# Kernel tuning notes

Measured on AMD Instinct MI355X. Metric: run time of the kernel, lower is better.

Reference implementation:

```python
import jax, jax.numpy as jnp
import numpy as np

NUM_HEADS = 8

def conv1x1(x, w, b):
    # x: [B,C,H,W], w: [O,C], b: [O]
    return jnp.einsum('bchw,oc->bohw', x, w) + b[None, :, None, None]

def setup_inputs() -> dict:
    key = jax.random.key(0)
    ks = jax.random.split(key, 8)
    B, C, H, W = 8, 256, 32, 32
    HF, WF = 128, 128
    s = 1.0 / np.sqrt(C)  # xavier-ish scale for 1x1 convs
    return {
        'x': jax.random.normal(ks[0], (B, C, H, W), jnp.float32),
        'featmap': jax.random.normal(ks[1], (B, C, HF, WF), jnp.float32),
        'wq': jax.random.normal(ks[2], (C, C), jnp.float32) * s,
        'bq': jnp.zeros((C,), jnp.float32),
        'wk': jax.random.normal(ks[3], (C, C), jnp.float32) * s,
        'bk': jnp.zeros((C,), jnp.float32),
        'wv': jax.random.normal(ks[4], (C, C), jnp.float32) * s,
        'bv': jnp.zeros((C,), jnp.float32),
        'wg': jax.random.normal(ks[5], (1, C), jnp.float32) * s,
        'bg': jnp.zeros((1,), jnp.float32),
    }

def _to_grid(t, h, w, rh, rw):
    # t: [B8, d, h*rh, w*rw] -> [B8, d, h, w, rh*rw] (aligned local grid per query pixel)
    b8, d = t.shape[:2]
    t = t.reshape(b8, d, h, rh, w, rw)
    return t.transpose(0, 1, 2, 4, 3, 5).reshape(b8, d, h, w, rh * rw)

def reference(x, featmap, wq, bq, wk, bk, wv, bv, wg, bg):
    B, C, H, W = x.shape
    HF, WF = featmap.shape[2:]
    head_dim = C // NUM_HEADS
    scaling = float(head_dim) ** -0.5
    rh, rw = HF // H, WF // W

    grid_weight = jax.nn.sigmoid(conv1x1(x, wg, bg))          # [B,1,H,W]
    q = conv1x1(x, wq, bq) * scaling                           # [B,C,H,W]
    k = conv1x1(featmap, wk, bk)                               # [B,C,HF,WF]
    v = conv1x1(featmap, wv, bv)

    q = q.reshape(B * NUM_HEADS, head_dim, H, W)
    k = k.reshape(B * NUM_HEADS, head_dim, HF, WF)
    v = v.reshape(B * NUM_HEADS, head_dim, HF, WF)

    k_grid = _to_grid(k, H, W, rh, rw)                         # [B8,d,H,W,P]
    v_grid = _to_grid(v, H, W, rh, rw)

    # ga_align_weight: correlate each query pixel with its aligned key grid
    attn = jnp.einsum('bchw,bchwp->bphw', q, k_grid)           # [B8,P,H,W]
    attn = jax.nn.softmax(attn, axis=1)
    # ga_align_map: weighted sum of aligned value grid
    out = jnp.einsum('bphw,bchwp->bchw', attn, v_grid)         # [B8,d,H,W]

    out = out.reshape(B, C, H, W) * grid_weight
    return out
```

## Files before the change

kernel.cpp:

```cpp
#include <hip/hip_runtime.h>

#define CDIM 256
#define SCALING 0.17677669529663687f

typedef _Float16 f16;
typedef f16 f16x4 __attribute__((ext_vector_type(4)));
typedef f16 f16x8 __attribute__((ext_vector_type(8)));
typedef float f32x4 __attribute__((ext_vector_type(4)));

#define MFMA(a, b, c) __builtin_amdgcn_mfma_f32_16x16x32_f16(a, b, c, 0, 0, 0)

__global__ __launch_bounds__(256) void k_prep_w2(const float* __restrict__ wq,
                                                 const float* __restrict__ bq,
                                                 const float* __restrict__ wk,
                                                 f16* __restrict__ W2h,
                                                 float* __restrict__ b2) {
  __shared__ float wk_s[32][8];
  const int t = threadIdx.x, ciO = blockIdx.x, hd = blockIdx.y;
  {
    int j = t >> 3, c8 = t & 7;
    wk_s[j][c8] = wk[(hd * 32 + j) * CDIM + ciO * 8 + c8];
  }
  float wq_r[32];
#pragma unroll
  for (int j = 0; j < 32; ++j) wq_r[j] = wq[(hd * 32 + j) * CDIM + t];
  __syncthreads();
  for (int c8 = 0; c8 < 8; ++c8) {
    float acc = 0.f;
#pragma unroll
    for (int j = 0; j < 32; ++j) acc = fmaf(wq_r[j], wk_s[j][c8], acc);
    W2h[(size_t)(hd * CDIM + ciO * 8 + c8) * CDIM + t] = (f16)(acc * SCALING);
  }
  if (t < 8) {
    float a = 0.f;
    for (int j = 0; j < 32; ++j) a = fmaf(wk_s[j][t], bq[hd * 32 + j], a);
    b2[hd * CDIM + ciO * 8 + t] = a * SCALING;
  }
}

__global__ __launch_bounds__(256) void k_cvt_wv(const float* __restrict__ wv,
                                                f16* __restrict__ wvh) {
  int i = (blockIdx.x * 256 + threadIdx.x) * 4;
  float4 v = *(const float4*)(wv + i);
  f16x4 h;
  h[0] = (f16)v.x; h[1] = (f16)v.y; h[2] = (f16)v.z; h[3] = (f16)v.w;
  *(f16x4*)(wvh + i) = h;
}

__global__ __launch_bounds__(256, 2) void k_qkw2(const float* __restrict__ x,
                                                 const f16* __restrict__ W2h,
                                                 const float* __restrict__ b2,
                                                 const float* __restrict__ wg,
                                                 const float* __restrict__ bg,
                                                 f16* __restrict__ qk,
                                                 float* __restrict__ gw, int b0) {
  __shared__ __align__(16) f16 A_l[256 * 40];
  __shared__ __align__(16) f16 B_l[64 * 40];
  const int t = threadIdx.x;
  const int p16 = blockIdx.x, hd = blockIdx.y, bz = blockIdx.z;
  const int bb = b0 + bz;
  const int lane = t & 63, wid = t >> 6, l15 = lane & 15, h4 = lane >> 4;
  f32x4 acc[4][4] = {};
  float gacc = 0.f;

  for (int kb = 0; kb < 8; ++kb) {
    __syncthreads();
#pragma unroll
    for (int it = 0; it < 4; ++it) {
      int e = it * 256 + t, ci = e >> 2, q = e & 3;
      *(f16x8*)(A_l + ci * 40 + q * 8) =
          *(const f16x8*)(W2h + (size_t)(hd * CDIM + ci) * CDIM + kb * 32 + q * 8);
    }
#pragma unroll
    for (int it = 0; it < 2; ++it) {
      int e = it * 256 + t, cx = e >> 4, p4 = e & 15;
      float4 v = *(const float4*)(x + (size_t)(bb * CDIM + kb * 32 + cx) * 1024 +
                                  p16 * 64 + p4 * 4);
      B_l[(p4 * 4 + 0) * 40 + cx] = (f16)v.x;
      B_l[(p4 * 4 + 1) * 40 + cx] = (f16)v.y;
      B_l[(p4 * 4 + 2) * 40 + cx] = (f16)v.z;
      B_l[(p4 * 4 + 3) * 40 + cx] = (f16)v.w;
    }
    __syncthreads();
    if (hd == 0 && wid == 3) {
#pragma unroll
      for (int cx = 0; cx < 32; ++cx)
        gacc = fmaf(wg[kb * 32 + cx], (float)B_l[lane * 40 + cx], gacc);
    }
    f16x8 a[4], bf[4];
#pragma unroll
    for (int mt = 0; mt < 4; ++mt)
      a[mt] = *(const f16x8*)(A_l + (wid * 64 + mt * 16 + l15) * 40 + h4 * 8);
#pragma unroll
    for (int nt = 0; nt < 4; ++nt)
      bf[nt] = *(const f16x8*)(B_l + (nt * 16 + l15) * 40 + h4 * 8);
#pragma unroll
    for (int mt = 0; mt < 4; ++mt)
#pragma unroll
      for (int nt = 0; nt < 4; ++nt) acc[mt][nt] = MFMA(a[mt], bf[nt], acc[mt][nt]);
  }
#pragma unroll
  for (int mt = 0; mt < 4; ++mt) {
    int ci0 = wid * 64 + mt * 16 + h4 * 4;
    float4 bvv = *(const float4*)(b2 + hd * CDIM + ci0);
#pragma unroll
    for (int nt = 0; nt < 4; ++nt) {
      int pix = p16 * 64 + nt * 16 + l15;
      union { f16 h[4]; unsigned long long u; } P;
      P.h[0] = (f16)(acc[mt][nt][0] + bvv.x);
      P.h[1] = (f16)(acc[mt][nt][1] + bvv.y);
      P.h[2] = (f16)(acc[mt][nt][2] + bvv.z);
      P.h[3] = (f16)(acc[mt][nt][3] + bvv.w);
      *(unsigned long long*)(qk + ((size_t)(bz * 1024 + pix) * 8 + hd) * CDIM + ci0) = P.u;
    }
  }
  if (hd == 0 && wid == 3)
    gw[bz * 1024 + p16 * 64 + lane] = 1.f / (1.f + __expf(-(gacc + bg[0])));
}

__global__ __launch_bounds__(256, 2) void k_attn(const float* __restrict__ feat,
                                                 const f16* __restrict__ qk,
                                                 f16* __restrict__ fa, int b0) {
  __shared__ __align__(16) f16 featb_cip[4 * 4128];
  __shared__ __align__(16) f16 featb_pci[4 * 4224];
  __shared__ __align__(16) f16 attn_l[4 * 16 * 32];
  const int t = threadIdx.x;
  const int h = blockIdx.x, w4 = blockIdx.y, bz = blockIdx.z;
  const int bb = b0 + bz;
  const int lane = t & 63, w = t >> 6, l15 = lane & 15, h4 = lane >> 4;
  const int pixb = h * 32 + w4 * 4;

  {
    f16x8 z = {};
    *(f16x8*)(attn_l + t * 8) = z;
  }
  if (t < 128) {
    int wi = t >> 5, i = t & 31;
    featb_cip[wi * 4128 + 4096 + i] = (f16)0;
  }
  const float* fb = feat + (size_t)bb * (CDIM * 16384) + (h * 4) * 128 + w4 * 16;
#pragma unroll
  for (int it = 0; it < 16; ++it) {
    int e = it * 256 + t, j4 = e & 3, r = (e >> 2) & 3, ci = e >> 4;
    float4 v = *(const float4*)(fb + (size_t)ci * 16384 + r * 128 + j4 * 4);
    f16x4 hv;
    hv[0] = (f16)v.x; hv[1] = (f16)v.y; hv[2] = (f16)v.z; hv[3] = (f16)v.w;
    *(f16x4*)(featb_cip + j4 * 4128 + ci * 16 + r * 4) = hv;
    int pb = j4 * 4224 + ci;
    featb_pci[pb + (r * 4 + 0) * 264] = hv[0];
    featb_pci[pb + (r * 4 + 1) * 264] = hv[1];
    featb_pci[pb + (r * 4 + 2) * 264] = hv[2];
    featb_pci[pb + (r * 4 + 3) * 264] = hv[3];
  }
  __syncthreads();

  const f16* qkg = qk + ((size_t)(bz * 1024 + pixb + w) * 8 + (l15 & 7)) * CDIM;
  const f16* fpci = featb_pci + w * 4224 + l15 * 264;
  f32x4 acc = {};
#pragma unroll
  for (int kb = 0; kb < 8; ++kb) {
    f16x8 a = *(const f16x8*)(qkg + kb * 32 + h4 * 8);
    f16x8 bf = *(const f16x8*)(fpci + kb * 32 + h4 * 8);
    acc = MFMA(a, bf, acc);
  }
  float at[4];
#pragma unroll
  for (int r = 0; r < 4; ++r) {
    float m = acc[r];
    m = fmaxf(m, __shfl_xor(m, 1, 64));
    m = fmaxf(m, __shfl_xor(m, 2, 64));
    m = fmaxf(m, __shfl_xor(m, 4, 64));
    m = fmaxf(m, __shfl_xor(m, 8, 64));
    float e = __expf(acc[r] - m);
    float s = e;
    s += __shfl_xor(s, 1, 64);
    s += __shfl_xor(s, 2, 64);
    s += __shfl_xor(s, 4, 64);
    s += __shfl_xor(s, 8, 64);
    at[r] = e / s;
  }
  if (h4 < 2) {
#pragma unroll
    for (int r = 0; r < 4; ++r) attn_l[(w * 16 + h4 * 4 + r) * 32 + l15] = (f16)at[r];
  }
  f16x8 bfr = *(const f16x8*)(attn_l + (w * 16 + l15) * 32 + h4 * 8);
  const f16* fw = featb_cip + w * 4128;
  f32x4 zero = {};
#pragma unroll
  for (int mt = 0; mt < 16; ++mt) {
    f16x8 a5 = *(const f16x8*)(fw + (mt * 16 + l15) * 16 + h4 * 8);
    f32x4 d = MFMA(a5, bfr, zero);
    if (l15 < 8) {
      int ci0 = mt * 16 + h4 * 4;
      union { f16 h[4]; unsigned long long u; } P;
      P.h[0] = (f16)d[0]; P.h[1] = (f16)d[1]; P.h[2] = (f16)d[2]; P.h[3] = (f16)d[3];
      *(unsigned long long*)(fa + ((size_t)(bz * 8 + l15) * 1024 + pixb + w) * CDIM + ci0) =
          P.u;
    }
  }
}

__global__ __launch_bounds__(256) void k_out(const f16* __restrict__ fa,
                                             const f16* __restrict__ wvh,
                                             const float* __restrict__ bv,
                                             const float* __restrict__ gw,
                                             float* __restrict__ out, int b0) {
  __shared__ __align__(16) f16 wv_l[32 * 264];
  __shared__ __align__(16) f16 fa_l[64 * 40];
  const int t = threadIdx.x;
  const int p16 = blockIdx.x, hd = blockIdx.y, bz = blockIdx.z;
  const int bb = b0 + bz;
  const int lane = t & 63, wid = t >> 6, l15 = lane & 15, h4 = lane >> 4;
#pragma unroll
  for (int it = 0; it < 4; ++it) {
    int e = it * 256 + t, c = e >> 5, ch = e & 31;
    *(f16x8*)(wv_l + c * 264 + ch * 8) =
        *(const f16x8*)(wvh + (size_t)(hd * 32 + c) * CDIM + ch * 8);
  }
  f32x4 acc[2] = {};
  for (int kb = 0; kb < 8; ++kb) {
    __syncthreads();
    {
      int pixl = t >> 2, q = t & 3;
      *(f16x8*)(fa_l + pixl * 40 + q * 8) =
          *(const f16x8*)(fa + ((size_t)(bz * 8 + hd) * 1024 + p16 * 64 + pixl) * CDIM +
                          kb * 32 + q * 8);
    }
    __syncthreads();
    f16x8 a = *(const f16x8*)(fa_l + (wid * 16 + l15) * 40 + h4 * 8);
#pragma unroll
    for (int nt = 0; nt < 2; ++nt) {
      f16x8 b = *(const f16x8*)(wv_l + (nt * 16 + l15) * 264 + kb * 32 + h4 * 8);
      acc[nt] = MFMA(a, b, acc[nt]);
    }
  }
  int pix0 = p16 * 64 + wid * 16 + h4 * 4;
  float4 g = *(const float4*)(gw + bz * 1024 + pix0);
#pragma unroll
  for (int nt = 0; nt < 2; ++nt) {
    int c = hd * 32 + nt * 16 + l15;
    float bvc = bv[c];
    float4 o;
    o.x = (acc[nt][0] + bvc) * g.x;
    o.y = (acc[nt][1] + bvc) * g.y;
    o.z = (acc[nt][2] + bvc) * g.z;
    o.w = (acc[nt][3] + bvc) * g.w;
    *(float4*)(out + (size_t)(bb * CDIM + c) * 1024 + pix0) = o;
  }
}

extern "C" void kernel_launch(void* const* d_in, const int* in_sizes, int n_in,
                              void* d_out, int out_size, void* d_ws, size_t ws_size,
                              hipStream_t stream) {
  const float* x = (const float*)d_in[0];
  const float* feat = (const float*)d_in[1];
  const float* wq = (const float*)d_in[2];
  const float* bq = (const float*)d_in[3];
  const float* wk = (const float*)d_in[4];
  const float* wv = (const float*)d_in[6];
  const float* bv = (const float*)d_in[7];
  const float* wg = (const float*)d_in[8];
  const float* bg = (const float*)d_in[9];
  float* out = (float*)d_out;

  char* ws = (char*)d_ws;
  f16* W2h = (f16*)ws;
  float* b2 = (float*)(ws + 1048576);
  f16* wvh = (f16*)(ws + 1056768);
  char* dyn = ws + 1187840;

  k_prep_w2<<<dim3(32, 8), 256, 0, stream>>>(wq, bq, wk, W2h, b2);
  k_cvt_wv<<<64, 256, 0, stream>>>(wv, wvh);

  const size_t QK = 4194304, FA = 4194304, GW = 4096;
  if (ws_size >= 1187840 + 8 * (QK + FA + GW)) {
    f16* qk = (f16*)dyn;
    f16* fa = (f16*)(dyn + 8 * QK);
    float* gwp = (float*)(dyn + 8 * (QK + FA));
    k_qkw2<<<dim3(16, 8, 8), 256, 0, stream>>>(x, W2h, b2, wg, bg, qk, gwp, 0);
    k_attn<<<dim3(32, 8, 8), 256, 0, stream>>>(feat, qk, fa, 0);
    k_out<<<dim3(16, 8, 8), 256, 0, stream>>>(fa, wvh, bv, gwp, out, 0);
  } else {
    f16* qk = (f16*)dyn;
    f16* fa = (f16*)(dyn + QK);
    float* gwp = (float*)(dyn + QK + FA);
    for (int b = 0; b < 8; ++b) {
      k_qkw2<<<dim3(16, 8, 1), 256, 0, stream>>>(x, W2h, b2, wg, bg, qk, gwp, b);
      k_attn<<<dim3(32, 8, 1), 256, 0, stream>>>(feat, qk, fa, b);
      k_out<<<dim3(16, 8, 1), 256, 0, stream>>>(fa, wvh, bv, gwp, out, b);
    }
  }
}
```

Baseline: 88.21 us.

## Fuse value projection into attention kernel and merge wv conversion into prep

The output 1x1 value projection (k_out) is folded into k_attn. The attention-weighted features stay in shared memory and are multiplied by the f16 wv weights straight from global memory, which removes the fa intermediate write and read round trip. The wv fp32-to-f16 conversion moves into k_prep_w2, which saves a launch. The cost is redundant wv weight reads per block, a strided scalar output store (only 4 lanes write per tile), and MFMA work with mostly idle rows, since only 4 pixels are used per 16-wide tile.

```diff
diff --git a/kernel.cpp b/kernel.cpp
--- a/kernel.cpp
+++ b/kernel.cpp
@@ -13,13 +13,17 @@
 __global__ __launch_bounds__(256) void k_prep_w2(const float* __restrict__ wq,
                                                  const float* __restrict__ bq,
                                                  const float* __restrict__ wk,
+                                                 const float* __restrict__ wv,
                                                  f16* __restrict__ W2h,
-                                                 float* __restrict__ b2) {
+                                                 float* __restrict__ b2,
+                                                 f16* __restrict__ wvh) {
   __shared__ float wk_s[32][8];
   const int t = threadIdx.x, ciO = blockIdx.x, hd = blockIdx.y;
   {
     int j = t >> 3, c8 = t & 7;
     wk_s[j][c8] = wk[(hd * 32 + j) * CDIM + ciO * 8 + c8];
+    int idx = (hd * 32 + j) * CDIM + ciO * 8 + c8;
+    wvh[idx] = (f16)wv[idx];
   }
   float wq_r[32];
 #pragma unroll
@@ -36,15 +40,6 @@
     for (int j = 0; j < 32; ++j) a = fmaf(wk_s[j][t], bq[hd * 32 + j], a);
     b2[hd * CDIM + ciO * 8 + t] = a * SCALING;
   }
-}
-
-__global__ __launch_bounds__(256) void k_cvt_wv(const float* __restrict__ wv,
-                                                f16* __restrict__ wvh) {
-  int i = (blockIdx.x * 256 + threadIdx.x) * 4;
-  float4 v = *(const float4*)(wv + i);
-  f16x4 h;
-  h[0] = (f16)v.x; h[1] = (f16)v.y; h[2] = (f16)v.z; h[3] = (f16)v.w;
-  *(f16x4*)(wvh + i) = h;
 }
 
 __global__ __launch_bounds__(256, 2) void k_qkw2(const float* __restrict__ x,
@@ -120,9 +115,12 @@
 
 __global__ __launch_bounds__(256, 2) void k_attn(const float* __restrict__ feat,
                                                  const f16* __restrict__ qk,
-                                                 f16* __restrict__ fa, int b0) {
+                                                 const f16* __restrict__ wvh,
+                                                 const float* __restrict__ bv,
+                                                 const float* __restrict__ gw,
+                                                 float* __restrict__ out, int b0) {
   __shared__ __align__(16) f16 featb_cip[4 * 4128];
-  __shared__ __align__(16) f16 featb_pci[4 * 4224];
+  __shared__ __align__(16) f16 smem2[4 * 4224];
   __shared__ __align__(16) f16 attn_l[4 * 16 * 32];
   const int t = threadIdx.x;
   const int h = blockIdx.x, w4 = blockIdx.y, bz = blockIdx.z;
@@ -147,15 +145,15 @@
     hv[0] = (f16)v.x; hv[1] = (f16)v.y; hv[2] = (f16)v.z; hv[3] = (f16)v.w;
     *(f16x4*)(featb_cip + j4 * 4128 + ci * 16 + r * 4) = hv;
     int pb = j4 * 4224 + ci;
-    featb_pci[pb + (r * 4 + 0) * 264] = hv[0];
-    featb_pci[pb + (r * 4 + 1) * 264] = hv[1];
-    featb_pci[pb + (r * 4 + 2) * 264] = hv[2];
-    featb_pci[pb + (r * 4 + 3) * 264] = hv[3];
+    smem2[pb + (r * 4 + 0) * 264] = hv[0];
+    smem2[pb + (r * 4 + 1) * 264] = hv[1];
+    smem2[pb + (r * 4 + 2) * 264] = hv[2];
+    smem2[pb + (r * 4 + 3) * 264] = hv[3];
   }
   __syncthreads();
 
   const f16* qkg = qk + ((size_t)(bz * 1024 + pixb + w) * 8 + (l15 & 7)) * CDIM;
-  const f16* fpci = featb_pci + w * 4224 + l15 * 264;
+  const f16* fpci = smem2 + w * 4224 + l15 * 264;
   f32x4 acc = {};
 #pragma unroll
   for (int kb = 0; kb < 8; ++kb) {
@@ -183,69 +181,51 @@
 #pragma unroll
     for (int r = 0; r < 4; ++r) attn_l[(w * 16 + h4 * 4 + r) * 32 + l15] = (f16)at[r];
   }
-  f16x8 bfr = *(const f16x8*)(attn_l + (w * 16 + l15) * 32 + h4 * 8);
-  const f16* fw = featb_cip + w * 4128;
-  f32x4 zero = {};
-#pragma unroll
-  for (int mt = 0; mt < 16; ++mt) {
-    f16x8 a5 = *(const f16x8*)(fw + (mt * 16 + l15) * 16 + h4 * 8);
-    f32x4 d = MFMA(a5, bfr, zero);
-    if (l15 < 8) {
-      int ci0 = mt * 16 + h4 * 4;
-      union { f16 h[4]; unsigned long long u; } P;
-      P.h[0] = (f16)d[0]; P.h[1] = (f16)d[1]; P.h[2] = (f16)d[2]; P.h[3] = (f16)d[3];
-      *(unsigned long long*)(fa + ((size_t)(bz * 8 + l15) * 1024 + pixb + w) * CDIM + ci0) =
-          P.u;
-    }
-  }
-}
-
-__global__ __launch_bounds__(256) void k_out(const f16* __restrict__ fa,
-                                             const f16* __restrict__ wvh,
-                                             const float* __restrict__ bv,
-                                             const float* __restrict__ gw,
-                                             float* __restrict__ out, int b0) {
-  __shared__ __align__(16) f16 wv_l[32 * 264];
-  __shared__ __align__(16) f16 fa_l[64 * 40];
-  const int t = threadIdx.x;
-  const int p16 = blockIdx.x, hd = blockIdx.y, bz = blockIdx.z;
-  const int bb = b0 + bz;
-  const int lane = t & 63, wid = t >> 6, l15 = lane & 15, h4 = lane >> 4;
-#pragma unroll
-  for (int it = 0; it < 4; ++it) {
-    int e = it * 256 + t, c = e >> 5, ch = e & 31;
-    *(f16x8*)(wv_l + c * 264 + ch * 8) =
-        *(const f16x8*)(wvh + (size_t)(hd * 32 + c) * CDIM + ch * 8);
-  }
-  f32x4 acc[2] = {};
-  for (int kb = 0; kb < 8; ++kb) {
-    __syncthreads();
-    {
-      int pixl = t >> 2, q = t & 3;
-      *(f16x8*)(fa_l + pixl * 40 + q * 8) =
-          *(const f16x8*)(fa + ((size_t)(bz * 8 + hd) * 1024 + p16 * 64 + pixl) * CDIM +
-                          kb * 32 + q * 8);
-    }
-    __syncthreads();
-    f16x8 a = *(const f16x8*)(fa_l + (wid * 16 + l15) * 40 + h4 * 8);
-#pragma unroll
-    for (int nt = 0; nt < 2; ++nt) {
-      f16x8 b = *(const f16x8*)(wv_l + (nt * 16 + l15) * 264 + kb * 32 + h4 * 8);
-      acc[nt] = MFMA(a, b, acc[nt]);
-    }
-  }
-  int pix0 = p16 * 64 + wid * 16 + h4 * 4;
-  float4 g = *(const float4*)(gw + bz * 1024 + pix0);
-#pragma unroll
-  for (int nt = 0; nt < 2; ++nt) {
-    int c = hd * 32 + nt * 16 + l15;
-    float bvc = bv[c];
-    float4 o;
-    o.x = (acc[nt][0] + bvc) * g.x;
-    o.y = (acc[nt][1] + bvc) * g.y;
-    o.z = (acc[nt][2] + bvc) * g.z;
-    o.w = (acc[nt][3] + bvc) * g.w;
-    *(float4*)(out + (size_t)(bb * CDIM + c) * 1024 + pix0) = o;
+  __syncthreads();
+
+  {
+    f16x8 afr = *(const f16x8*)(attn_l + (w * 16 + l15) * 32 + h4 * 8);
+    const f16* fw = featb_cip + w * 4128;
+    f32x4 zero = {};
+#pragma unroll
+    for (int nt = 0; nt < 16; ++nt) {
+      f16x8 b5 = *(const f16x8*)(fw + (nt * 16 + l15) * 16 + h4 * 8);
+      f32x4 d = MFMA(afr, b5, zero);
+      if (h4 < 2) {
+#pragma unroll
+        for (int r = 0; r < 4; ++r)
+          smem2[((h4 * 4 + r) * 4 + w) * 264 + nt * 16 + l15] = (f16)d[r];
+      }
+    }
+  }
+  __syncthreads();
+
+  {
+    const float gwv = gw[bz * 1024 + pixb + (l15 & 3)];
+#pragma unroll
+    for (int hd2 = 0; hd2 < 2; ++hd2) {
+      const int hd = w * 2 + hd2;
+#pragma unroll
+      for (int mt = 0; mt < 2; ++mt) {
+        f32x4 acc6 = {};
+#pragma unroll
+        for (int kb = 0; kb < 8; ++kb) {
+          f16x8 a6 = *(const f16x8*)(wvh + (size_t)(hd * 32 + mt * 16 + l15) * CDIM +
+                                     kb * 32 + h4 * 8);
+          f16x8 b6 = *(const f16x8*)(smem2 + (hd * 4 + (l15 & 3)) * 264 + kb * 32 + h4 * 8);
+          acc6 = MFMA(a6, b6, acc6);
+        }
+        if (l15 < 4) {
+          float4 bv4 = *(const float4*)(bv + hd * 32 + mt * 16 + h4 * 4);
+          const int c0 = hd * 32 + mt * 16 + h4 * 4;
+#pragma unroll
+          for (int r = 0; r < 4; ++r) {
+            float o = (acc6[r] + ((const float*)&bv4)[r]) * gwv;
+            out[(size_t)(bb * CDIM + c0 + r) * 1024 + pixb + l15] = o;
+          }
+        }
+      }
+    }
   }
 }
 
@@ -269,25 +249,20 @@
   f16* wvh = (f16*)(ws + 1056768);
   char* dyn = ws + 1187840;
 
-  k_prep_w2<<<dim3(32, 8), 256, 0, stream>>>(wq, bq, wk, W2h, b2);
-  k_cvt_wv<<<64, 256, 0, stream>>>(wv, wvh);
-
-  const size_t QK = 4194304, FA = 4194304, GW = 4096;
-  if (ws_size >= 1187840 + 8 * (QK + FA + GW)) {
+  k_prep_w2<<<dim3(32, 8), 256, 0, stream>>>(wq, bq, wk, wv, W2h, b2, wvh);
+
+  const size_t QK = 4194304, GW = 4096;
+  if (ws_size >= 1187840 + 8 * (QK + GW)) {
     f16* qk = (f16*)dyn;
-    f16* fa = (f16*)(dyn + 8 * QK);
-    float* gwp = (float*)(dyn + 8 * (QK + FA));
+    float* gwp = (float*)(dyn + 8 * QK);
     k_qkw2<<<dim3(16, 8, 8), 256, 0, stream>>>(x, W2h, b2, wg, bg, qk, gwp, 0);
-    k_attn<<<dim3(32, 8, 8), 256, 0, stream>>>(feat, qk, fa, 0);
-    k_out<<<dim3(16, 8, 8), 256, 0, stream>>>(fa, wvh, bv, gwp, out, 0);
+    k_attn<<<dim3(32, 8, 8), 256, 0, stream>>>(feat, qk, wvh, bv, gwp, out, 0);
   } else {
     f16* qk = (f16*)dyn;
-    f16* fa = (f16*)(dyn + QK);
-    float* gwp = (float*)(dyn + QK + FA);
+    float* gwp = (float*)(dyn + QK);
     for (int b = 0; b < 8; ++b) {
       k_qkw2<<<dim3(16, 8, 1), 256, 0, stream>>>(x, W2h, b2, wg, bg, qk, gwp, b);
-      k_attn<<<dim3(32, 8, 1), 256, 0, stream>>>(feat, qk, fa, b);
-      k_out<<<dim3(16, 8, 1), 256, 0, stream>>>(fa, wvh, bv, gwp, out, b);
-    }
-  }
-}
+      k_attn<<<dim3(32, 8, 1), 256, 0, stream>>>(feat, qk, wvh, bv, gwp, out, b);
+    }
+  }
+}
```

Result: slower. 102.8 us (+16.5%).

## Store featmap tile once in padded LDS layout and fold wv conversion into prep

Applied to the files above, without the earlier changes.

The attention kernel previously kept two fp16 copies of the feature tile in LDS, one channel-major and one pixel-major. It now keeps a single channel-major copy with an 18-element row stride and gathers the MFMA B operand with strided scalar LDS reads. This halves LDS use and allows launch bounds of 4 blocks per CU. The wv fp16 conversion is merged into the weight-prep kernel, removing one launch. The trade-off is more, narrower LDS reads per MFMA and possible bank conflicts on the gathered loads.

```diff
diff --git a/kernel.cpp b/kernel.cpp
--- a/kernel.cpp
+++ b/kernel.cpp
@@ -10,16 +10,27 @@
 
 #define MFMA(a, b, c) __builtin_amdgcn_mfma_f32_16x16x32_f16(a, b, c, 0, 0, 0)
 
+__device__ __forceinline__ unsigned pack2(float a, float b) {
+  union { f16 h[2]; unsigned u; } r;
+  r.h[0] = (f16)a;
+  r.h[1] = (f16)b;
+  return r.u;
+}
+
 __global__ __launch_bounds__(256) void k_prep_w2(const float* __restrict__ wq,
                                                  const float* __restrict__ bq,
                                                  const float* __restrict__ wk,
+                                                 const float* __restrict__ wv,
                                                  f16* __restrict__ W2h,
-                                                 float* __restrict__ b2) {
+                                                 float* __restrict__ b2,
+                                                 f16* __restrict__ wvh) {
   __shared__ float wk_s[32][8];
   const int t = threadIdx.x, ciO = blockIdx.x, hd = blockIdx.y;
   {
     int j = t >> 3, c8 = t & 7;
     wk_s[j][c8] = wk[(hd * 32 + j) * CDIM + ciO * 8 + c8];
+    int idx = (hd * 32 + j) * CDIM + ciO * 8 + c8;
+    wvh[idx] = (f16)wv[idx];
   }
   float wq_r[32];
 #pragma unroll
@@ -36,15 +47,6 @@
     for (int j = 0; j < 32; ++j) a = fmaf(wk_s[j][t], bq[hd * 32 + j], a);
     b2[hd * CDIM + ciO * 8 + t] = a * SCALING;
   }
-}
-
-__global__ __launch_bounds__(256) void k_cvt_wv(const float* __restrict__ wv,
-                                                f16* __restrict__ wvh) {
-  int i = (blockIdx.x * 256 + threadIdx.x) * 4;
-  float4 v = *(const float4*)(wv + i);
-  f16x4 h;
-  h[0] = (f16)v.x; h[1] = (f16)v.y; h[2] = (f16)v.z; h[3] = (f16)v.w;
-  *(f16x4*)(wvh + i) = h;
 }
 
 __global__ __launch_bounds__(256, 2) void k_qkw2(const float* __restrict__ x,
@@ -118,12 +120,11 @@
     gw[bz * 1024 + p16 * 64 + lane] = 1.f / (1.f + __expf(-(gacc + bg[0])));
 }
 
-__global__ __launch_bounds__(256, 2) void k_attn(const float* __restrict__ feat,
+__global__ __launch_bounds__(256, 4) void k_attn(const float* __restrict__ feat,
                                                  const f16* __restrict__ qk,
                                                  f16* __restrict__ fa, int b0) {
-  __shared__ __align__(16) f16 featb_cip[4 * 4128];
-  __shared__ __align__(16) f16 featb_pci[4 * 4224];
-  __shared__ __align__(16) f16 attn_l[4 * 16 * 32];
+  __shared__ __align__(16) f16 cip[4 * 4608];
+  __shared__ __align__(16) f16 attn_l[4 * 512];
   const int t = threadIdx.x;
   const int h = blockIdx.x, w4 = blockIdx.y, bz = blockIdx.z;
   const int bb = b0 + bz;
@@ -134,33 +135,31 @@
     f16x8 z = {};
     *(f16x8*)(attn_l + t * 8) = z;
   }
-  if (t < 128) {
-    int wi = t >> 5, i = t & 31;
-    featb_cip[wi * 4128 + 4096 + i] = (f16)0;
+#pragma unroll
+  for (int it = 0; it < 4; ++it) {
+    int e = it * 256 + t, px = e >> 8, ci = e & 255;
+    *(unsigned*)(cip + px * 4608 + ci * 18 + 16) = 0;
   }
   const float* fb = feat + (size_t)bb * (CDIM * 16384) + (h * 4) * 128 + w4 * 16;
 #pragma unroll
   for (int it = 0; it < 16; ++it) {
-    int e = it * 256 + t, j4 = e & 3, r = (e >> 2) & 3, ci = e >> 4;
-    float4 v = *(const float4*)(fb + (size_t)ci * 16384 + r * 128 + j4 * 4);
-    f16x4 hv;
-    hv[0] = (f16)v.x; hv[1] = (f16)v.y; hv[2] = (f16)v.z; hv[3] = (f16)v.w;
-    *(f16x4*)(featb_cip + j4 * 4128 + ci * 16 + r * 4) = hv;
-    int pb = j4 * 4224 + ci;
-    featb_pci[pb + (r * 4 + 0) * 264] = hv[0];
-    featb_pci[pb + (r * 4 + 1) * 264] = hv[1];
-    featb_pci[pb + (r * 4 + 2) * 264] = hv[2];
-    featb_pci[pb + (r * 4 + 3) * 264] = hv[3];
+    int e = it * 256 + t, px = e & 3, r = (e >> 2) & 3, ci = e >> 4;
+    float4 v = *(const float4*)(fb + (size_t)ci * 16384 + r * 128 + px * 4);
+    unsigned* d = (unsigned*)(cip + px * 4608 + ci * 18 + r * 4);
+    d[0] = pack2(v.x, v.y);
+    d[1] = pack2(v.z, v.w);
   }
   __syncthreads();
 
   const f16* qkg = qk + ((size_t)(bz * 1024 + pixb + w) * 8 + (l15 & 7)) * CDIM;
-  const f16* fpci = featb_pci + w * 4224 + l15 * 264;
+  const f16* cw = cip + w * 4608;
   f32x4 acc = {};
 #pragma unroll
   for (int kb = 0; kb < 8; ++kb) {
     f16x8 a = *(const f16x8*)(qkg + kb * 32 + h4 * 8);
-    f16x8 bf = *(const f16x8*)(fpci + kb * 32 + h4 * 8);
+    f16x8 bf;
+#pragma unroll
+    for (int j = 0; j < 8; ++j) bf[j] = cw[(kb * 32 + h4 * 8 + j) * 18 + l15];
     acc = MFMA(a, bf, acc);
   }
   float at[4];
@@ -181,21 +180,23 @@
   }
   if (h4 < 2) {
 #pragma unroll
-    for (int r = 0; r < 4; ++r) attn_l[(w * 16 + h4 * 4 + r) * 32 + l15] = (f16)at[r];
-  }
-  f16x8 bfr = *(const f16x8*)(attn_l + (w * 16 + l15) * 32 + h4 * 8);
-  const f16* fw = featb_cip + w * 4128;
-  f32x4 zero = {};
-#pragma unroll
-  for (int mt = 0; mt < 16; ++mt) {
-    f16x8 a5 = *(const f16x8*)(fw + (mt * 16 + l15) * 16 + h4 * 8);
-    f32x4 d = MFMA(a5, bfr, zero);
+    for (int r = 0; r < 4; ++r) attn_l[w * 512 + l15 * 16 + h4 * 4 + r] = (f16)at[r];
+  }
+  f16x8 b5;
+#pragma unroll
+  for (int j = 0; j < 8; ++j) b5[j] = attn_l[w * 512 + (h4 * 8 + j) * 16 + l15];
+  const f32x4 zero = {};
+#pragma unroll
+  for (int nt = 0; nt < 16; ++nt) {
+    const unsigned* ap = (const unsigned*)(cw + (nt * 16 + l15) * 18 + h4 * 8);
+    union { unsigned u[4]; f16x8 h; } A;
+    A.u[0] = ap[0]; A.u[1] = ap[1]; A.u[2] = ap[2]; A.u[3] = ap[3];
+    f32x4 d = MFMA(A.h, b5, zero);
     if (l15 < 8) {
-      int ci0 = mt * 16 + h4 * 4;
       union { f16 h[4]; unsigned long long u; } P;
       P.h[0] = (f16)d[0]; P.h[1] = (f16)d[1]; P.h[2] = (f16)d[2]; P.h[3] = (f16)d[3];
-      *(unsigned long long*)(fa + ((size_t)(bz * 8 + l15) * 1024 + pixb + w) * CDIM + ci0) =
-          P.u;
+      *(unsigned long long*)(fa + ((size_t)(bz * 8 + l15) * 1024 + pixb + w) * CDIM +
+                             nt * 16 + h4 * 4) = P.u;
     }
   }
 }
@@ -269,25 +270,24 @@
   f16* wvh = (f16*)(ws + 1056768);
   char* dyn = ws + 1187840;
 
-  k_prep_w2<<<dim3(32, 8), 256, 0, stream>>>(wq, bq, wk, W2h, b2);
-  k_cvt_wv<<<64, 256, 0, stream>>>(wv, wvh);
+  k_prep_w2<<<dim3(32, 8), 256, 0, stream>>>(wq, bq, wk, wv, W2h, b2, wvh);
 
   const size_t QK = 4194304, FA = 4194304, GW = 4096;
   if (ws_size >= 1187840 + 8 * (QK + FA + GW)) {
-    f16* qk = (f16*)dyn;
-    f16* fa = (f16*)(dyn + 8 * QK);
+    f16* qkp = (f16*)dyn;
+    f16* fap = (f16*)(dyn + 8 * QK);
     float* gwp = (float*)(dyn + 8 * (QK + FA));
-    k_qkw2<<<dim3(16, 8, 8), 256, 0, stream>>>(x, W2h, b2, wg, bg, qk, gwp, 0);
-    k_attn<<<dim3(32, 8, 8), 256, 0, stream>>>(feat, qk, fa, 0);
-    k_out<<<dim3(16, 8, 8), 256, 0, stream>>>(fa, wvh, bv, gwp, out, 0);
+    k_qkw2<<<dim3(16, 8, 8), 256, 0, stream>>>(x, W2h, b2, wg, bg, qkp, gwp, 0);
+    k_attn<<<dim3(32, 8, 8), 256, 0, stream>>>(feat, qkp, fap, 0);
+    k_out<<<dim3(16, 8, 8), 256, 0, stream>>>(fap, wvh, bv, gwp, out, 0);
   } else {
-    f16* qk = (f16*)dyn;
-    f16* fa = (f16*)(dyn + QK);
+    f16* qkp = (f16*)dyn;
+    f16* fap = (f16*)(dyn + QK);
     float* gwp = (float*)(dyn + QK + FA);
     for (int b = 0; b < 8; ++b) {
-      k_qkw2<<<dim3(16, 8, 1), 256, 0, stream>>>(x, W2h, b2, wg, bg, qk, gwp, b);
-      k_attn<<<dim3(32, 8, 1), 256, 0, stream>>>(feat, qk, fa, b);
-      k_out<<<dim3(16, 8, 1), 256, 0, stream>>>(fa, wvh, bv, gwp, out, b);
-    }
-  }
-}
+      k_qkw2<<<dim3(16, 8, 1), 256, 0, stream>>>(x, W2h, b2, wg, bg, qkp, gwp, b);
+      k_attn<<<dim3(32, 8, 1), 256, 0, stream>>>(feat, qkp, fap, b);
+      k_out<<<dim3(16, 8, 1), 256, 0, stream>>>(fap, wvh, bv, gwp, out, b);
+    }
+  }
+}
```

Result: faster. 80.35 us (-8.9%).
